# Optimization experiments

Hardware: AMD Instinct MI355X
Metric: run time of the kernel (lower is better)

The kernel has to match this reference:

```python
import jax, jax.numpy as jnp
import numpy as np

B, S, V, E, HID = 16, 40, 1004, 256, 256
C, R, HW = 1024, 256, 32  # featureChannel, releMapChannel, spatial
BN_EPS = 1e-5


def setup_inputs() -> dict:
    key = jax.random.key(0)
    ks = jax.random.split(key, 16)
    sc = 0.05
    emb = jax.random.normal(ks[4], (V, E), jnp.float32) * sc
    emb = emb.at[0].set(0.0)  # padding_idx = 0
    return {
        "feature": jax.random.normal(ks[0], (B, C, HW, HW), jnp.float32),
        "depth": jax.random.uniform(ks[1], (B, 1, HW, HW), jnp.float32),
        "instruction_idx": jax.random.randint(ks[2], (B, S), 0, V, jnp.int32),
        "instruction_length": jnp.clip(jax.random.randint(ks[3], (B,), 1, S + 1, jnp.int32), 1, S),
        "only_train_rele": 1,
        "emb_table": emb,
        "w_ih": jax.random.normal(ks[5], (4 * HID, E), jnp.float32) * sc,
        "w_hh": jax.random.normal(ks[6], (4 * HID, HID), jnp.float32) * sc,
        "b_ih": jax.random.normal(ks[7], (4 * HID,), jnp.float32) * sc,
        "b_hh": jax.random.normal(ks[8], (4 * HID,), jnp.float32) * sc,
        "e2d_w": jax.random.normal(ks[9], (HID, HID), jnp.float32) * sc,
        "e2d_b": jax.random.normal(ks[10], (HID,), jnp.float32) * sc,
        "lin1_w": jax.random.normal(ks[11], (R * C, HID), jnp.float32) * sc,
        "lin1_b": jax.random.normal(ks[12], (R * C,), jnp.float32) * sc,
        "bn_gamma": jnp.ones((R,), jnp.float32),
        "bn_beta": jnp.zeros((R,), jnp.float32),
        "bn_mean": jax.random.normal(ks[13], (R,), jnp.float32) * 0.01,
        "bn_var": jnp.ones((R,), jnp.float32),
    }


def _encoder_lstm(idx, lengths, emb_table, w_ih, w_hh, b_ih, b_hh, e2d_w, e2d_b):
    # Faithful to packed-sequence LSTM: state stops updating at each sample's length.
    embeds = emb_table[idx]                      # [B,S,E]
    xs = jnp.swapaxes(embeds, 0, 1)              # [S,B,E]
    mask = (jnp.arange(S)[:, None] < lengths[None, :])  # [S,B]
    h0 = jnp.zeros((B, HID), embeds.dtype)
    c0 = jnp.zeros((B, HID), embeds.dtype)

    def step(carry, xm):
        h, c = carry
        x_t, m = xm                              # [B,E], [B]
        gates = x_t @ w_ih.T + h @ w_hh.T + (b_ih + b_hh)  # [B,4H]
        i, f, g, o = jnp.split(gates, 4, axis=-1)  # torch gate order: i,f,g,o
        c_new = jax.nn.sigmoid(f) * c + jax.nn.sigmoid(i) * jnp.tanh(g)
        h_new = jax.nn.sigmoid(o) * jnp.tanh(c_new)
        m = m[:, None]
        return (jnp.where(m, h_new, h), jnp.where(m, c_new, c)), None

    (h_t, _), _ = jax.lax.scan(step, (h0, c0), (xs, mask))
    return jnp.tanh(h_t @ e2d_w.T + e2d_b)       # [B,HID]


def reference(feature, depth, instruction_idx, instruction_length, only_train_rele,
              emb_table, w_ih, w_hh, b_ih, b_hh, e2d_w, e2d_b,
              lin1_w, lin1_b, bn_gamma, bn_beta, bn_mean, bn_var):
    instr = _encoder_lstm(instruction_idx, instruction_length, emb_table,
                          w_ih, w_hh, b_ih, b_hh, e2d_w, e2d_b)  # [B,HID]
    # per-sample dynamic 1x1 filters (dropout in eval mode -> identity)
    f1 = jax.nn.leaky_relu(instr @ lin1_w.T + lin1_b, negative_slope=0.01)
    f1 = f1.reshape(B, R, C)
    # batched per-sample 1x1 conv: one einsum replaces the batch loop of F.conv2d
    rele = jax.nn.relu(jnp.einsum('bchw,brc->brhw', feature, f1))  # [B,R,H,W]
    # BatchNorm2d in eval mode with running stats
    scale = bn_gamma / jnp.sqrt(bn_var + BN_EPS)
    rele = rele * scale[None, :, None, None] + (bn_beta - bn_mean * scale)[None, :, None, None]
    single = jnp.max(rele, axis=1)               # channel-max pooling -> [B,H,W]
    return jnp.clip(single, 0.0, 1.0)
```

## Files before the change

kernel.cpp:

```cpp
#include <hip/hip_runtime.h>
#include <hip/hip_fp16.h>
#include <math.h>

#define NB 16
#define SQ 40
#define HIDN 256
#define CC 1024
#define NROW 262144

#define AGENT __HIP_MEMORY_SCOPE_AGENT
#define SENT 0x7E7E7E7Eu

__device__ __forceinline__ float sigf(float x){ return 1.0f/(1.0f+__expf(-x)); }

typedef _Float16 h2v __attribute__((ext_vector_type(2)));
typedef _Float16 f16x8 __attribute__((ext_vector_type(8)));
typedef float    f32x4 __attribute__((ext_vector_type(4)));

__device__ __forceinline__ float fd2(unsigned w, unsigned h, float acc){
  h2v a = __builtin_bit_cast(h2v, w);
  h2v b = __builtin_bit_cast(h2v, h);
#if __has_builtin(__builtin_amdgcn_fdot2)
  return __builtin_amdgcn_fdot2(a, b, acc, false);
#else
  return acc + (float)a.x*(float)b.x + (float)a.y*(float)b.y;
#endif
}

__device__ __forceinline__ unsigned pkh(float lo, float hi){
  return (unsigned)__half_as_ushort(__float2half_rn(lo))
       | ((unsigned)__half_as_ushort(__float2half_rn(hi)) << 16);
}

__global__ __launch_bounds__(256) void k_xgates(
    const int* __restrict__ idx, const float* __restrict__ emb,
    const float* __restrict__ w_ih, const float* __restrict__ b_ih,
    const float* __restrict__ b_hh, float* __restrict__ XG)
{
  __shared__ float xs[8*256];
  int t = threadIdx.x;
  int tb0 = blockIdx.x * 8;
  #pragma unroll
  for (int i = 0; i < 8; ++i) {
    int flat = t + i*256;
    int p = flat >> 8, k = flat & 255;
    int tb = tb0 + p;
    int ts = tb >> 4, b = tb & 15;
    int row = idx[b*SQ + ts];
    xs[p*256 + k] = emb[row*256 + k];
  }
  __syncthreads();
  int rows[4];
  float acc[4][8];
  #pragma unroll
  for (int r = 0; r < 4; ++r) {
    rows[r] = t + r*256;
    float bias = b_ih[rows[r]] + b_hh[rows[r]];
    #pragma unroll
    for (int p = 0; p < 8; ++p) acc[r][p] = bias;
  }
  for (int k16 = 0; k16 < 16; ++k16) {
    float4 w[4][4];
    #pragma unroll
    for (int r = 0; r < 4; ++r)
      #pragma unroll
      for (int q = 0; q < 4; ++q)
        w[r][q] = *(const float4*)&w_ih[rows[r]*256 + k16*16 + q*4];
    #pragma unroll
    for (int p = 0; p < 8; ++p) {
      #pragma unroll
      for (int q = 0; q < 4; ++q) {
        float4 x = *(const float4*)&xs[p*256 + k16*16 + q*4];
        #pragma unroll
        for (int r = 0; r < 4; ++r)
          acc[r][p] += w[r][q].x*x.x + w[r][q].y*x.y + w[r][q].z*x.z + w[r][q].w*x.w;
      }
    }
  }
  #pragma unroll
  for (int p = 0; p < 8; ++p)
    #pragma unroll
    for (int r = 0; r < 4; ++r)
      XG[(tb0 + p)*1024 + rows[r]] = acc[r][p];
}

__global__ __launch_bounds__(256) void k_whh3(const float* __restrict__ w, unsigned* __restrict__ W3)
{
  int tid = blockIdx.x*256 + threadIdx.x;
  int c    = tid & 3;
  int tt   = (tid >> 2) & 511;
  int q    = (tid >> 11) & 31;
  int half = tid >> 16;
  int pair = 4*q + c;
  int g = tt >> 7, j = tt & 127;
  int row = g*256 + half*128 + j;
  float2 v = *(const float2*)&w[(size_t)row*256 + 2*pair];
  W3[tid] = pkh(v.x, v.y);
}

__global__ __launch_bounds__(512) void k_lstm2(
    const float* __restrict__ XG, const uint4* __restrict__ W3,
    const int* __restrict__ lens, const float* __restrict__ e2d_w,
    const float* __restrict__ e2d_b, float* __restrict__ instr,
    unsigned* __restrict__ hcomm)
{
  __shared__ float dot_s[512];
  __shared__ float h_s[128];
  __shared__ float h_e[256];

  int t = threadIdx.x;
  int b    = blockIdx.x & 15;
  int half = blockIdx.x >> 4;
  int len  = lens[b];
  int lane = t & 63;

  unsigned wv[128];
  {
    const uint4* wp = W3 + (size_t)half*32*512 + t;
    #pragma unroll
    for (int q = 0; q < 32; ++q) {
      uint4 v = wp[(size_t)q*512];
      wv[4*q+0]=v.x; wv[4*q+1]=v.y; wv[4*q+2]=v.z; wv[4*q+3]=v.w;
    }
  }

  int g = t >> 7, j = t & 127;
  int row = g*256 + half*128 + j;
  float c_reg = 0.0f, h_reg = 0.0f;

  float xg_cur = XG[(0*NB + b)*1024 + row];

  for (int it = 0; it < SQ; ++it) {
    float xg_next = (it+1 < SQ) ? XG[((it+1)*NB + b)*1024 + row] : 0.0f;
    float acc = xg_cur;
    if (it > 0) {
      unsigned own = pkh(h_s[2*lane], h_s[2*lane + 1]);
      int owni = (int)own;
      const unsigned* oslot = hcomm + ((it-1)*NB + b)*128 + (half ? 0 : 64);
      if (half == 0) {
        #pragma unroll
        for (int q = 0; q < 64; ++q)
          acc = fd2(wv[q], (unsigned)__builtin_amdgcn_readlane(owni, q), acc);
        unsigned oth;
        do { oth = __hip_atomic_load(oslot + lane, __ATOMIC_RELAXED, AGENT); }
        while (__any((int)(oth == SENT)));
        int othi = (int)oth;
        #pragma unroll
        for (int q = 0; q < 64; ++q)
          acc = fd2(wv[64+q], (unsigned)__builtin_amdgcn_readlane(othi, q), acc);
      } else {
        #pragma unroll
        for (int q = 0; q < 64; ++q)
          acc = fd2(wv[64+q], (unsigned)__builtin_amdgcn_readlane(owni, q), acc);
        unsigned oth;
        do { oth = __hip_atomic_load(oslot + lane, __ATOMIC_RELAXED, AGENT); }
        while (__any((int)(oth == SENT)));
        int othi = (int)oth;
        #pragma unroll
        for (int q = 0; q < 64; ++q)
          acc = fd2(wv[q], (unsigned)__builtin_amdgcn_readlane(othi, q), acc);
      }
    }
    dot_s[t] = acc;
    __syncthreads();
    if (t < 128) {
      float iv = sigf (dot_s[t]);
      float fv = sigf (dot_s[t + 128]);
      float gv = tanhf(dot_s[t + 256]);
      float ov = sigf (dot_s[t + 384]);
      float cn = fv*c_reg + iv*gv;
      float hn = ov*tanhf(cn);
      if (it < len) { c_reg = cn; h_reg = hn; }
      h_s[t] = h_reg;
    }
    __syncthreads();
    if (t < 64)
      __hip_atomic_store(hcomm + (it*NB + b)*128 + half*64 + t,
                         pkh(h_s[2*t], h_s[2*t+1]), __ATOMIC_RELAXED, AGENT);
    xg_cur = xg_next;
  }

  if (half == 0) {
    const unsigned* slot = hcomm + ((SQ-1)*NB + b)*128;
    if (t < 64) {
      unsigned v0, v1;
      do {
        v0 = __hip_atomic_load(slot + t,      __ATOMIC_RELAXED, AGENT);
        v1 = __hip_atomic_load(slot + 64 + t, __ATOMIC_RELAXED, AGENT);
      } while (__any((int)(v0 == SENT)) || __any((int)(v1 == SENT)));
      h2v lo = __builtin_bit_cast(h2v, v0);
      h2v hi = __builtin_bit_cast(h2v, v1);
      h_e[2*t]       = (float)lo.x;  h_e[2*t + 1]       = (float)lo.y;
      h_e[128 + 2*t] = (float)hi.x;  h_e[128 + 2*t + 1] = (float)hi.y;
    }
    __syncthreads();
    if (t < 256) {
      float acc2 = e2d_b[t];
      const float4* wp2 = (const float4*)&e2d_w[t*256];
      #pragma unroll 8
      for (int k4 = 0; k4 < 64; ++k4) {
        float4 w = wp2[k4];
        float4 h4 = *(const float4*)&h_e[k4*4];
        acc2 += w.x*h4.x + w.y*h4.y + w.z*h4.z + w.w*h4.w;
      }
      instr[b*256 + t] = tanhf(acc2);
    }
  }
}

__global__ __launch_bounds__(256) void k_lin1(
    const float* __restrict__ instr, const float* __restrict__ w,
    const float* __restrict__ bias, _Float16* __restrict__ f1h)
{
  __shared__ float is[4096];
  int t = threadIdx.x;
  #pragma unroll
  for (int i = 0; i < 16; ++i) is[t + i*256] = instr[t + i*256];
  __syncthreads();
  int r0 = blockIdx.x*256 + t;
  const float* w0 = &w[(size_t)r0*256];
  float acc0[16];
  float bz0 = bias[r0];
  #pragma unroll
  for (int i = 0; i < 16; ++i) acc0[i] = bz0;
  for (int k16 = 0; k16 < 16; ++k16) {
    float4 a[4];
    #pragma unroll
    for (int q = 0; q < 4; ++q)
      a[q] = *(const float4*)&w0[k16*16 + q*4];
    #pragma unroll
    for (int bi = 0; bi < 16; ++bi) {
      #pragma unroll
      for (int q = 0; q < 4; ++q) {
        float4 x = *(const float4*)&is[bi*256 + k16*16 + q*4];
        acc0[bi] += a[q].x*x.x + a[q].y*x.y + a[q].z*x.z + a[q].w*x.w;
      }
    }
  }
  #pragma unroll
  for (int bi = 0; bi < 16; ++bi) {
    float v0 = acc0[bi]; v0 = v0 > 0.0f ? v0 : 0.01f*v0;
    f1h[(size_t)bi*NROW + r0] = (_Float16)v0;
  }
}

__global__ __launch_bounds__(256, 1) void k_einsum_mfma(
    const uint4* __restrict__ f1h4, const float* __restrict__ feat,
    const float* __restrict__ gamma, const float* __restrict__ beta,
    const float* __restrict__ mean, const float* __restrict__ var,
    float* __restrict__ out)
{
  __shared__ unsigned ALDS[256*20];
  __shared__ unsigned BLDS[64*20];
  __shared__ float sc_s[256], sh_s[256];
  __shared__ float red[4][64];

  int t = threadIdx.x;
  int b  = blockIdx.x >> 4;
  int P0 = (blockIdx.x & 15) * 64;
  int wr = t >> 6, lane = t & 63;
  int col = lane & 15, quad = lane >> 4;

  {
    float s = gamma[t] * rsqrtf(var[t] + 1e-5f);
    sc_s[t] = s;
    sh_s[t] = beta[t] - mean[t]*s;
  }

  f32x4 acc[4][4];
  #pragma unroll
  for (int mt = 0; mt < 4; ++mt)
    #pragma unroll
    for (int nt = 0; nt < 4; ++nt) acc[mt][nt] = (f32x4)0.0f;

  const uint4* arow = f1h4 + ((size_t)b*NROW + (size_t)t*1024)/8;
  int p_loc = t & 63, kq = t >> 6;
  const float* bbase = feat + ((size_t)b*1024 + kq*8)*1024 + P0 + p_loc;

  uint4 apf[4];
  float bpf[8];
  #pragma unroll
  for (int g = 0; g < 4; ++g) apf[g] = arow[g];
  #pragma unroll
  for (int j = 0; j < 8; ++j) bpf[j] = bbase[(size_t)j*1024];

  for (int kc = 0; kc < 32; ++kc) {
    __syncthreads();
    #pragma unroll
    for (int g = 0; g < 4; ++g)
      *(uint4*)&ALDS[t*20 + g*4] = apf[g];
    {
      unsigned u[4];
      #pragma unroll
      for (int c = 0; c < 4; ++c) u[c] = pkh(bpf[2*c], bpf[2*c+1]);
      uint4 w0 = {u[0],u[1],u[2],u[3]};
      *(uint4*)&BLDS[p_loc*20 + kq*4] = w0;
    }
    __syncthreads();
    if (kc + 1 < 32) {
      #pragma unroll
      for (int g = 0; g < 4; ++g) apf[g] = arow[(kc+1)*4 + g];
      const float* bb = bbase + (size_t)(kc+1)*32*1024;
      #pragma unroll
      for (int j = 0; j < 8; ++j) bpf[j] = bb[(size_t)j*1024];
    }
    f16x8 bf[4];
    #pragma unroll
    for (int nt = 0; nt < 4; ++nt) {
      uint4 raw = *(const uint4*)&BLDS[(nt*16 + col)*20 + quad*4];
      bf[nt] = __builtin_bit_cast(f16x8, raw);
    }
    #pragma unroll
    for (int mt = 0; mt < 4; ++mt) {
      uint4 raw = *(const uint4*)&ALDS[(wr*64 + mt*16 + col)*20 + quad*4];
      f16x8 af = __builtin_bit_cast(f16x8, raw);
      #pragma unroll
      for (int nt = 0; nt < 4; ++nt)
        acc[mt][nt] = __builtin_amdgcn_mfma_f32_16x16x32_f16(af, bf[nt], acc[mt][nt], 0, 0, 0);
    }
  }

  float pmax[4];
  #pragma unroll
  for (int nt = 0; nt < 4; ++nt) pmax[nt] = -3.4e38f;
  #pragma unroll
  for (int mt = 0; mt < 4; ++mt) {
    int rb = wr*64 + mt*16 + quad*4;
    f32x4 scv = *(const f32x4*)&sc_s[rb];
    f32x4 shv = *(const f32x4*)&sh_s[rb];
    #pragma unroll
    for (int nt = 0; nt < 4; ++nt) {
      f32x4 a = acc[mt][nt];
      #pragma unroll
      for (int reg = 0; reg < 4; ++reg) {
        float v = fmaxf(a[reg], 0.0f)*scv[reg] + shv[reg];
        pmax[nt] = fmaxf(pmax[nt], v);
      }
    }
  }
  #pragma unroll
  for (int nt = 0; nt < 4; ++nt) {
    float m = pmax[nt];
    m = fmaxf(m, __shfl_xor(m, 16));
    m = fmaxf(m, __shfl_xor(m, 32));
    if (lane < 16) red[wr][nt*16 + lane] = m;
  }
  __syncthreads();
  if (t < 64) {
    float v = fmaxf(fmaxf(red[0][t], red[1][t]), fmaxf(red[2][t], red[3][t]));
    out[b*1024 + P0 + t] = fminf(fmaxf(v, 0.0f), 1.0f);
  }
}

extern "C" void kernel_launch(void* const* d_in, const int* in_sizes, int n_in,
                              void* d_out, int out_size, void* d_ws, size_t ws_size,
                              hipStream_t stream)
{
  const float* feature = (const float*)d_in[0];
  const int*   idx     = (const int*)d_in[2];
  const int*   lens    = (const int*)d_in[3];
  const float* emb     = (const float*)d_in[5];
  const float* w_ih    = (const float*)d_in[6];
  const float* w_hh    = (const float*)d_in[7];
  const float* b_ih    = (const float*)d_in[8];
  const float* b_hh    = (const float*)d_in[9];
  const float* e2d_w   = (const float*)d_in[10];
  const float* e2d_b   = (const float*)d_in[11];
  const float* lin1_w  = (const float*)d_in[12];
  const float* lin1_b  = (const float*)d_in[13];
  const float* gamma   = (const float*)d_in[14];
  const float* beta    = (const float*)d_in[15];
  const float* mean    = (const float*)d_in[16];
  const float* var     = (const float*)d_in[17];

  char* ws = (char*)d_ws;
  float*    XG     = (float*)(ws);
  float*    instr  = (float*)(ws + 2621440);
  unsigned* W3     = (unsigned*)(ws + 2637824);
  unsigned* hcomm  = (unsigned*)(ws + 3162112);
  _Float16* f1h    = (_Float16*)(ws + 3489792);

  hipMemsetAsync(hcomm, 0x7E, 327680, stream);
  k_xgates <<<80,   256, 0, stream>>>(idx, emb, w_ih, b_ih, b_hh, XG);
  k_whh3   <<<512,  256, 0, stream>>>(w_hh, W3);
  k_lstm2  <<<32,   512, 0, stream>>>(XG, (const uint4*)W3, lens, e2d_w, e2d_b, instr, hcomm);
  k_lin1   <<<1024, 256, 0, stream>>>(instr, lin1_w, lin1_b, f1h);
  k_einsum_mfma <<<256, 256, 0, stream>>>((const uint4*)f1h, feature, gamma, beta, mean, var,
                                          (float*)d_out);
}
```

Measured before the change: 601.0 us.

## Overlap feature fp16 transpose with LSTM and merge prep kernels

Merges the x-gates and W_hh packing kernels into one launch. Adds extra blocks to the LSTM kernel that convert the 64 MB fp32 feature tensor to a transposed fp16 layout, so this conversion runs concurrently with the latency-bound serial LSTM on otherwise idle CUs. The einsum kernel then reads contiguous fp16 B rows with a larger K chunk (64 instead of 32), halving loop iterations and syncs and avoiding per-iteration fp32-to-fp16 packing. The cost is an extra 32 MB intermediate write and read, plus possible interference with the LSTM's inter-block communication because the LSTM blocks now share the GPU with the transpose blocks.

Result: no change. 610.4 us (+1.6%).

```diff
diff --git a/kernel.cpp b/kernel.cpp
--- a/kernel.cpp
+++ b/kernel.cpp
@@ -32,13 +32,27 @@
        | ((unsigned)__half_as_ushort(__float2half_rn(hi)) << 16);
 }
 
-__global__ __launch_bounds__(256) void k_xgates(
+__global__ __launch_bounds__(256) void k_prep(
     const int* __restrict__ idx, const float* __restrict__ emb,
     const float* __restrict__ w_ih, const float* __restrict__ b_ih,
-    const float* __restrict__ b_hh, float* __restrict__ XG)
+    const float* __restrict__ b_hh, float* __restrict__ XG,
+    const float* __restrict__ w_hh, unsigned* __restrict__ W3)
 {
   __shared__ float xs[8*256];
   int t = threadIdx.x;
+  if (blockIdx.x >= 80) {
+    int tid = (blockIdx.x - 80)*256 + t;
+    int c    = tid & 3;
+    int tt   = (tid >> 2) & 511;
+    int q    = (tid >> 11) & 31;
+    int half = tid >> 16;
+    int pair = 4*q + c;
+    int g = tt >> 7, j = tt & 127;
+    int row = g*256 + half*128 + j;
+    float2 v = *(const float2*)&w_hh[(size_t)row*256 + 2*pair];
+    W3[tid] = pkh(v.x, v.y);
+    return;
+  }
   int tb0 = blockIdx.x * 8;
   #pragma unroll
   for (int i = 0; i < 8; ++i) {
@@ -84,31 +98,48 @@
       XG[(tb0 + p)*1024 + rows[r]] = acc[r][p];
 }
 
-__global__ __launch_bounds__(256) void k_whh3(const float* __restrict__ w, unsigned* __restrict__ W3)
-{
-  int tid = blockIdx.x*256 + threadIdx.x;
-  int c    = tid & 3;
-  int tt   = (tid >> 2) & 511;
-  int q    = (tid >> 11) & 31;
-  int half = tid >> 16;
-  int pair = 4*q + c;
-  int g = tt >> 7, j = tt & 127;
-  int row = g*256 + half*128 + j;
-  float2 v = *(const float2*)&w[(size_t)row*256 + 2*pair];
-  W3[tid] = pkh(v.x, v.y);
-}
-
-__global__ __launch_bounds__(512) void k_lstm2(
+__global__ __launch_bounds__(512) void k_lstm_ft(
     const float* __restrict__ XG, const uint4* __restrict__ W3,
     const int* __restrict__ lens, const float* __restrict__ e2d_w,
     const float* __restrict__ e2d_b, float* __restrict__ instr,
-    unsigned* __restrict__ hcomm)
+    unsigned* __restrict__ hcomm,
+    const float* __restrict__ feat, _Float16* __restrict__ fT)
 {
-  __shared__ float dot_s[512];
-  __shared__ float h_s[128];
-  __shared__ float h_e[256];
+  __shared__ __align__(16) char smem[73728];
 
   int t = threadIdx.x;
+
+  if (blockIdx.x >= 32) {
+    int sub = t >> 8, t2 = t & 255;
+    int tile = (blockIdx.x - 32)*2 + sub;
+    int b  = tile >> 6;
+    int rem = tile & 63;
+    int c0 = (rem >> 2) * 64;
+    int p0 = (rem & 3) * 256;
+    _Float16* tl = (_Float16*)smem + (size_t)sub*(256*72);
+    const float* src = feat + ((size_t)b*1024 + c0)*1024 + p0;
+    int wv2 = t2 >> 6, l = t2 & 63;
+    #pragma unroll
+    for (int i = 0; i < 16; ++i) {
+      int ci = i*4 + wv2;
+      float4 v = *(const float4*)&src[(size_t)ci*1024 + 4*l];
+      tl[(4*l + 0)*72 + ci] = (_Float16)v.x;
+      tl[(4*l + 1)*72 + ci] = (_Float16)v.y;
+      tl[(4*l + 2)*72 + ci] = (_Float16)v.z;
+      tl[(4*l + 3)*72 + ci] = (_Float16)v.w;
+    }
+    __syncthreads();
+    uint4* dst = (uint4*)&fT[((size_t)b*1024 + p0 + t2)*1024 + c0];
+    #pragma unroll
+    for (int j = 0; j < 8; ++j)
+      dst[j] = *(const uint4*)&tl[t2*72 + j*8];
+    return;
+  }
+
+  float* dot_s = (float*)smem;
+  float* h_s   = dot_s + 512;
+  float* h_e   = h_s + 128;
+
   int b    = blockIdx.x & 15;
   int half = blockIdx.x >> 4;
   int len  = lens[b];
@@ -244,20 +275,20 @@
   }
 }
 
-__global__ __launch_bounds__(256, 1) void k_einsum_mfma(
-    const uint4* __restrict__ f1h4, const float* __restrict__ feat,
+__global__ __launch_bounds__(256, 1) void k_einsum_fT(
+    const uint4* __restrict__ f1h4, const _Float16* __restrict__ fT,
     const float* __restrict__ gamma, const float* __restrict__ beta,
     const float* __restrict__ mean, const float* __restrict__ var,
     float* __restrict__ out)
 {
-  __shared__ unsigned ALDS[256*20];
-  __shared__ unsigned BLDS[64*20];
+  __shared__ unsigned ALDS[256*40];
+  __shared__ unsigned BLDS[64*40];
   __shared__ float sc_s[256], sh_s[256];
   __shared__ float red[4][64];
 
   int t = threadIdx.x;
-  int b  = blockIdx.x >> 4;
-  int P0 = (blockIdx.x & 15) * 64;
+  int b  = blockIdx.x & 15;
+  int P0 = (blockIdx.x >> 4) * 64;
   int wr = t >> 6, lane = t & 63;
   int col = lane & 15, quad = lane >> 4;
 
@@ -274,50 +305,47 @@
     for (int nt = 0; nt < 4; ++nt) acc[mt][nt] = (f32x4)0.0f;
 
   const uint4* arow = f1h4 + ((size_t)b*NROW + (size_t)t*1024)/8;
-  int p_loc = t & 63, kq = t >> 6;
-  const float* bbase = feat + ((size_t)b*1024 + kq*8)*1024 + P0 + p_loc;
-
-  uint4 apf[4];
-  float bpf[8];
-  #pragma unroll
-  for (int g = 0; g < 4; ++g) apf[g] = arow[g];
-  #pragma unroll
-  for (int j = 0; j < 8; ++j) bpf[j] = bbase[(size_t)j*1024];
-
-  for (int kc = 0; kc < 32; ++kc) {
-    __syncthreads();
-    #pragma unroll
-    for (int g = 0; g < 4; ++g)
-      *(uint4*)&ALDS[t*20 + g*4] = apf[g];
-    {
-      unsigned u[4];
-      #pragma unroll
-      for (int c = 0; c < 4; ++c) u[c] = pkh(bpf[2*c], bpf[2*c+1]);
-      uint4 w0 = {u[0],u[1],u[2],u[3]};
-      *(uint4*)&BLDS[p_loc*20 + kq*4] = w0;
-    }
-    __syncthreads();
-    if (kc + 1 < 32) {
-      #pragma unroll
-      for (int g = 0; g < 4; ++g) apf[g] = arow[(kc+1)*4 + g];
-      const float* bb = bbase + (size_t)(kc+1)*32*1024;
-      #pragma unroll
-      for (int j = 0; j < 8; ++j) bpf[j] = bb[(size_t)j*1024];
-    }
-    f16x8 bf[4];
-    #pragma unroll
-    for (int nt = 0; nt < 4; ++nt) {
-      uint4 raw = *(const uint4*)&BLDS[(nt*16 + col)*20 + quad*4];
-      bf[nt] = __builtin_bit_cast(f16x8, raw);
-    }
-    #pragma unroll
-    for (int mt = 0; mt < 4; ++mt) {
-      uint4 raw = *(const uint4*)&ALDS[(wr*64 + mt*16 + col)*20 + quad*4];
-      f16x8 af = __builtin_bit_cast(f16x8, raw);
-      #pragma unroll
-      for (int nt = 0; nt < 4; ++nt)
-        acc[mt][nt] = __builtin_amdgcn_mfma_f32_16x16x32_f16(af, bf[nt], acc[mt][nt], 0, 0, 0);
-    }
+  int p_loc = t >> 2, sub = t & 3;
+  const uint4* brow = (const uint4*)(fT + ((size_t)b*1024 + P0 + p_loc)*1024);
+
+  uint4 apf[8], bpf[2];
+  #pragma unroll
+  for (int g2 = 0; g2 < 8; ++g2) apf[g2] = arow[g2];
+  bpf[0] = brow[sub*2];
+  bpf[1] = brow[sub*2 + 1];
+
+  for (int kc = 0; kc < 16; ++kc) {
+    __syncthreads();
+    #pragma unroll
+    for (int g2 = 0; g2 < 8; ++g2)
+      *(uint4*)&ALDS[t*40 + g2*4] = apf[g2];
+    *(uint4*)&BLDS[p_loc*40 + sub*8]     = bpf[0];
+    *(uint4*)&BLDS[p_loc*40 + sub*8 + 4] = bpf[1];
+    __syncthreads();
+    if (kc + 1 < 16) {
+      #pragma unroll
+      for (int g2 = 0; g2 < 8; ++g2) apf[g2] = arow[(kc+1)*8 + g2];
+      bpf[0] = brow[(kc+1)*8 + sub*2];
+      bpf[1] = brow[(kc+1)*8 + sub*2 + 1];
+    }
+    f16x8 bf[2][4];
+    #pragma unroll
+    for (int s = 0; s < 2; ++s)
+      #pragma unroll
+      for (int nt = 0; nt < 4; ++nt) {
+        uint4 raw = *(const uint4*)&BLDS[(nt*16 + col)*40 + s*16 + quad*4];
+        bf[s][nt] = __builtin_bit_cast(f16x8, raw);
+      }
+    #pragma unroll
+    for (int s = 0; s < 2; ++s)
+      #pragma unroll
+      for (int mt = 0; mt < 4; ++mt) {
+        uint4 raw = *(const uint4*)&ALDS[(wr*64 + mt*16 + col)*40 + s*16 + quad*4];
+        f16x8 af = __builtin_bit_cast(f16x8, raw);
+        #pragma unroll
+        for (int nt = 0; nt < 4; ++nt)
+          acc[mt][nt] = __builtin_amdgcn_mfma_f32_16x16x32_f16(af, bf[s][nt], acc[mt][nt], 0, 0, 0);
+      }
   }
 
   float pmax[4];
@@ -379,12 +407,13 @@
   unsigned* W3     = (unsigned*)(ws + 2637824);
   unsigned* hcomm  = (unsigned*)(ws + 3162112);
   _Float16* f1h    = (_Float16*)(ws + 3489792);
+  _Float16* fT     = (_Float16*)(ws + 11878400);
 
   hipMemsetAsync(hcomm, 0x7E, 327680, stream);
-  k_xgates <<<80,   256, 0, stream>>>(idx, emb, w_ih, b_ih, b_hh, XG);
-  k_whh3   <<<512,  256, 0, stream>>>(w_hh, W3);
-  k_lstm2  <<<32,   512, 0, stream>>>(XG, (const uint4*)W3, lens, e2d_w, e2d_b, instr, hcomm);
+  k_prep   <<<592,  256, 0, stream>>>(idx, emb, w_ih, b_ih, b_hh, XG, w_hh, W3);
+  k_lstm_ft<<<544,  512, 0, stream>>>(XG, (const uint4*)W3, lens, e2d_w, e2d_b, instr, hcomm,
+                                      feature, fT);
   k_lin1   <<<1024, 256, 0, stream>>>(instr, lin1_w, lin1_b, f1h);
-  k_einsum_mfma <<<256, 256, 0, stream>>>((const uint4*)f1h, feature, gamma, beta, mean, var,
-                                          (float*)d_out);
-}
+  k_einsum_fT<<<256, 256, 0, stream>>>((const uint4*)f1h, fT, gamma, beta, mean, var,
+                                       (float*)d_out);
+}
```
